# Performance work log

Measured on AMD Instinct MI355X. Metric: run time of the kernel, lower is better.

Reference implementation:

```python
import jax, jax.numpy as jnp
import numpy as np

B, SEQ, DIM = 2, 2048, 1024
HEADS, HEAD_DIM = 16, 64
HIDDEN = 2816
EPS = 1e-5
LN_EPS = 1e-5


def rmsnorm(x, w, eps=EPS):
    return x * jax.lax.rsqrt(jnp.mean(x * x, axis=-1, keepdims=True) + eps) * w


def layernorm(x, w, b, eps=LN_EPS):
    mu = jnp.mean(x, axis=-1, keepdims=True)
    var = jnp.mean((x - mu) ** 2, axis=-1, keepdims=True)
    return (x - mu) * jax.lax.rsqrt(var + eps) * w + b


def modulate(x, shift, scale):
    # x: [B,S,D], shift/scale: [B,D]
    return x * (1.0 + scale[:, None, :]) + shift[:, None, :]


def apply_rope(t, cos, sin):
    # t: [B,S,H,D]; cos/sin: [S, D/2] -> complex multiply on (even,odd) pairs
    t = t.reshape(*t.shape[:-1], HEAD_DIM // 2, 2)
    t0, t1 = t[..., 0], t[..., 1]
    c = cos[None, :, None, :]
    s = sin[None, :, None, :]
    o0 = t0 * c - t1 * s
    o1 = t0 * s + t1 * c
    return jnp.stack([o0, o1], axis=-1).reshape(*t.shape[:-2], HEAD_DIM)


def setup_inputs() -> dict:
    key = jax.random.key(0)
    ks = jax.random.split(key, 12)
    def w(k, shape, s=0.02):
        return jax.random.normal(k, shape, dtype=jnp.float32) * s
    x = jax.random.normal(ks[0], (B, SEQ, DIM), dtype=jnp.float32)
    adaln_input = jax.random.normal(ks[1], (B, DIM), dtype=jnp.float32)
    pos = jnp.arange(SEQ, dtype=jnp.float32)
    inv_freq = 1.0 / (10000.0 ** (jnp.arange(0, HEAD_DIM, 2, dtype=jnp.float32) / HEAD_DIM))
    ang = pos[:, None] * inv_freq[None, :]  # [S, D/2]
    return dict(
        x=x, adaln_input=adaln_input,
        freqs_cos=jnp.cos(ang), freqs_sin=jnp.sin(ang),
        wq=w(ks[2], (DIM, DIM)), wk=w(ks[3], (DIM, DIM)),
        wv=w(ks[4], (DIM, DIM)), wo=w(ks[5], (DIM, DIM)),
        q_norm_w=jnp.ones(DIM, jnp.float32), q_norm_b=jnp.zeros(DIM, jnp.float32),
        k_norm_w=jnp.ones(DIM, jnp.float32), k_norm_b=jnp.zeros(DIM, jnp.float32),
        attn_norm_w=jnp.ones(DIM, jnp.float32), ffn_norm_w=jnp.ones(DIM, jnp.float32),
        ada_w=w(ks[6], (DIM, 6 * DIM)), ada_b=jnp.zeros(6 * DIM, jnp.float32),
        w1=w(ks[7], (DIM, HIDDEN)), w2=w(ks[8], (HIDDEN, DIM)), w3=w(ks[9], (DIM, HIDDEN)),
    )


def reference(x, adaln_input, freqs_cos, freqs_sin, wq, wk, wv, wo,
              q_norm_w, q_norm_b, k_norm_w, k_norm_b,
              attn_norm_w, ffn_norm_w, ada_w, ada_b, w1, w2, w3):
    # adaLN modulation: SiLU -> Linear -> 6 chunks of [B, DIM]
    m = jax.nn.silu(adaln_input) @ ada_w + ada_b
    shift_msa, scale_msa, gate_msa, shift_mlp, scale_mlp, gate_mlp = jnp.split(m, 6, axis=1)

    # --- attention branch ---
    h = modulate(rmsnorm(x, attn_norm_w), shift_msa, scale_msa)
    xq = layernorm(h @ wq, q_norm_w, q_norm_b)
    xk = layernorm(h @ wk, k_norm_w, k_norm_b)
    xv = h @ wv
    xq = xq.reshape(B, SEQ, HEADS, HEAD_DIM)
    xk = xk.reshape(B, SEQ, HEADS, HEAD_DIM)
    xv = xv.reshape(B, SEQ, HEADS, HEAD_DIM)
    xq = apply_rope(xq, freqs_cos, freqs_sin)
    xk = apply_rope(xk, freqs_cos, freqs_sin)
    scale = 1.0 / jnp.sqrt(jnp.float32(HEAD_DIM))
    scores = jnp.einsum('bshd,bthd->bhst', xq, xk) * scale  # [B,H,S,S]
    probs = jax.nn.softmax(scores, axis=-1)
    attn = jnp.einsum('bhst,bthd->bshd', probs, xv).reshape(B, SEQ, DIM)
    attn = attn @ wo
    x = x + gate_msa[:, None, :] * attn

    # --- MLP branch (SwiGLU) ---
    h = modulate(rmsnorm(x, ffn_norm_w), shift_mlp, scale_mlp)
    ffn = (jax.nn.silu(h @ w1) * (h @ w3)) @ w2
    x = x + gate_mlp[:, None, :] * ffn
    return x
```

## Files before the change

kernel.cpp:

```cpp
#include <hip/hip_runtime.h>
#include <hip/hip_bf16.h>

#define B_   2
#define S_   2048
#define D_   1024
#define H_   16
#define HD_  64
#define HID_ 2816

typedef unsigned short u16;
typedef unsigned int   u32;
typedef __attribute__((ext_vector_type(8))) short short8;
typedef __attribute__((ext_vector_type(4))) float f32x4;
typedef __attribute__((ext_vector_type(4))) u32   u32x4;

static __device__ __forceinline__ float bf2f(u16 u){ return __uint_as_float(((u32)u)<<16); }
static __device__ __forceinline__ u16 f2bf(float f){
  u32 u = __float_as_uint(f);
  u32 r = (u + 0x7FFFu + ((u>>16)&1u)) >> 16;
  return (u16)r;
}
static __device__ __forceinline__ u16 f2bfr(float f){
  return (u16)((__float_as_uint(f) + 0x8000u) >> 16);
}
static __device__ __forceinline__ u32 pk2(float a, float b){
  return ((__float_as_uint(a) + 0x8000u) >> 16) | ((__float_as_uint(b) + 0x8000u) & 0xFFFF0000u);
}

static __device__ __forceinline__ void ld4(const u16* p, float* v){
  ushort4 t = *reinterpret_cast<const ushort4*>(p);
  v[0]=bf2f(t.x); v[1]=bf2f(t.y); v[2]=bf2f(t.z); v[3]=bf2f(t.w);
}
static __device__ __forceinline__ void ld4(const float* p, float* v){
  float4 t = *reinterpret_cast<const float4*>(p);
  v[0]=t.x; v[1]=t.y; v[2]=t.z; v[3]=t.w;
}
static __device__ __forceinline__ void st4(u16* p, const float* v){
  ushort4 t; t.x=f2bf(v[0]); t.y=f2bf(v[1]); t.z=f2bf(v[2]); t.w=f2bf(v[3]);
  *reinterpret_cast<ushort4*>(p)=t;
}

static __device__ __forceinline__ float ld1g(const void* p, size_t i, bool f32){
  return f32 ? ((const float*)p)[i] : bf2f(((const u16*)p)[i]);
}
static __device__ __forceinline__ void ld4g(const void* p, size_t i, float* v, bool f32){
  if(f32){
    float4 t = *reinterpret_cast<const float4*>((const float*)p + i);
    v[0]=t.x; v[1]=t.y; v[2]=t.z; v[3]=t.w;
  }else{
    ushort4 t = *reinterpret_cast<const ushort4*>((const u16*)p + i);
    v[0]=bf2f(t.x); v[1]=bf2f(t.y); v[2]=bf2f(t.z); v[3]=bf2f(t.w);
  }
}
static __device__ __forceinline__ void st4g(void* p, size_t i, const float* v, bool f32){
  if(f32){
    float4 t; t.x=v[0]; t.y=v[1]; t.z=v[2]; t.w=v[3];
    *reinterpret_cast<float4*>((float*)p + i) = t;
  }else{
    st4((u16*)p + i, v);
  }
}

static __device__ __forceinline__ void gl2lds16(const u16* g, const u16* l){
  typedef __attribute__((address_space(3))) u16 lds_u16;
  typedef const __attribute__((address_space(1))) u16 glb_u16;
  __builtin_amdgcn_global_load_lds((glb_u16*)(uintptr_t)g,
                                   (lds_u16*)(u32)(uintptr_t)l, 16, 0, 0);
}

__global__ __launch_bounds__(256) void k_probe_zero(const u16* fc_raw, int* flag, float* m){
  int i = blockIdx.x*256 + threadIdx.x;
  if(i < 12288) m[i] = 0.f;
  if(i == 0) *flag = (fc_raw[0]==0) ? 1 : 0;
}

static __device__ __forceinline__ float blk_sum(float v, float* red){
  #pragma unroll
  for(int o=32;o;o>>=1) v += __shfl_xor(v,o,64);
  int lane = threadIdx.x & 63, w = threadIdx.x >> 6;
  if(lane==0) red[w]=v;
  __syncthreads();
  float t = red[0]+red[1]+red[2]+red[3];
  __syncthreads();
  return t;
}

__global__ __launch_bounds__(256) void k_adaln(const void* a, const void* W, const void* bias,
                                               float* m, const int* flag){
  bool f32 = flag[0] != 0;
  __shared__ float sl[2][128];
  int bk = blockIdx.y;
  {
    int bb = threadIdx.x >> 7, kk = threadIdx.x & 127;
    float x = ld1g(a, bb*D_ + bk*128 + kk, f32);
    sl[bb][kk] = x/(1.f+__expf(-x));
  }
  __syncthreads();
  int n = blockIdx.x*256 + threadIdx.x;
  float p0 = 0.f, p1 = 0.f;
  for(int kk=0;kk<128;kk++){
    float w = ld1g(W, (size_t)(bk*128+kk)*6144 + n, f32);
    p0 += sl[0][kk]*w; p1 += sl[1][kk]*w;
  }
  if(bk==0){ float bv = ld1g(bias, n, f32); p0 += bv; p1 += bv; }
  atomicAdd(&m[n], p0);
  atomicAdd(&m[6144+n], p1);
}

__global__ __launch_bounds__(256) void k_rms_mod(const void* x, const void* nw, const float* m,
                                                 u16* h, int shift_off, int scale_off,
                                                 const int* flag){
  bool f32 = flag[0] != 0;
  __shared__ float red[4];
  int row = blockIdx.x; int b = row >> 11;
  int d0 = threadIdx.x*4;
  float v[4]; ld4g(x, (size_t)row*D_ + d0, v, f32);
  float ss = v[0]*v[0]+v[1]*v[1]+v[2]*v[2]+v[3]*v[3];
  float tot = blk_sum(ss, red);
  float r = rsqrtf(tot*(1.f/D_) + 1e-5f);
  const float* mb = m + b*6144;
  float wn[4]; ld4g(nw, d0, wn, f32);
  float o[4];
  #pragma unroll
  for(int j=0;j<4;j++){
    int d = d0+j;
    o[j] = v[j]*r*wn[j]*(1.f+mb[scale_off+d]) + mb[shift_off+d];
  }
  st4(h + (size_t)row*D_ + d0, o);
}

__global__ __launch_bounds__(256) void k_resid_rms(const void* x, const u16* y, const float* m,
                                                   const void* nw, float* x2, u16* h,
                                                   const int* flag){
  bool f32 = flag[0] != 0;
  __shared__ float red[4];
  int row = blockIdx.x; int b = row >> 11;
  int d0 = threadIdx.x*4;
  size_t i4 = (size_t)row*D_ + d0;
  float xv[4], yv[4];
  ld4g(x, i4, xv, f32); ld4(y+i4, yv);
  const float* mb = m + b*6144;
  float v[4];
  #pragma unroll
  for(int j=0;j<4;j++) v[j] = xv[j] + mb[2048+d0+j]*yv[j];
  float4 t; t.x=v[0]; t.y=v[1]; t.z=v[2]; t.w=v[3];
  *reinterpret_cast<float4*>(x2+i4) = t;
  float ss = v[0]*v[0]+v[1]*v[1]+v[2]*v[2]+v[3]*v[3];
  float tot = blk_sum(ss, red);
  float r = rsqrtf(tot*(1.f/D_) + 1e-5f);
  float wn[4]; ld4g(nw, d0, wn, f32);
  float o[4];
  #pragma unroll
  for(int j=0;j<4;j++)
    o[j] = v[j]*r*wn[j]*(1.f+mb[4096+d0+j]) + mb[3072+d0+j];
  st4(h + i4, o);
}

__global__ __launch_bounds__(256) void k_ln_rope2(u16* t, const void* qw, const void* qb,
                                                  const void* kw, const void* kb2,
                                                  const void* fc, const void* fs, const int* flag){
  bool f32 = flag[0] != 0;
  __shared__ float red[4];
  int row = blockIdx.x; int s = row & (S_-1);
  const void* w  = blockIdx.y ? kw  : qw;
  const void* bb = blockIdx.y ? kb2 : qb;
  int d0 = threadIdx.x*4;
  u16* tp = t + (size_t)row*3072 + blockIdx.y*1024 + d0;
  float v[4]; ld4(tp, v);
  float sm = v[0]+v[1]+v[2]+v[3];
  float sq = v[0]*v[0]+v[1]*v[1]+v[2]*v[2]+v[3]*v[3];
  float tsm = blk_sum(sm, red);
  float tsq = blk_sum(sq, red);
  float mu  = tsm*(1.f/D_);
  float var = tsq*(1.f/D_) - mu*mu;
  float rs  = rsqrtf(var + 1e-5f);
  float wv[4], bv[4]; ld4g(w, d0, wv, f32); ld4g(bb, d0, bv, f32);
  float y[4];
  #pragma unroll
  for(int j=0;j<4;j++) y[j] = (v[j]-mu)*rs*wv[j] + bv[j];
  int pos = d0 & 63; int i0 = pos>>1;
  float c0 = ld1g(fc, s*32+i0,   f32), s0 = ld1g(fs, s*32+i0,   f32);
  float c1 = ld1g(fc, s*32+i0+1, f32), s1 = ld1g(fs, s*32+i0+1, f32);
  float o[4];
  o[0] = y[0]*c0 - y[1]*s0;
  o[1] = y[0]*s0 + y[1]*c0;
  o[2] = y[2]*c1 - y[3]*s1;
  o[3] = y[2]*s1 + y[3]*c1;
  st4(tp, o);
}

__global__ __launch_bounds__(256) void k_wt3(const void* W0, const void* W1, const void* W2,
                                             u16* WT, int Kd, int Nd, const int* flag){
  bool f32 = flag[0] != 0;
  const void* W = blockIdx.z==0 ? W0 : (blockIdx.z==1 ? W1 : W2);
  u16* dst_base = WT + (size_t)blockIdx.z * (size_t)Kd * Nd;
  __shared__ u16 L[64][72];
  int tid = threadIdx.x;
  int k0 = blockIdx.x*64, n0 = blockIdx.y*64;
  int r = tid>>2, c0 = (tid&3)*16;
  if(f32){
    const float* Wf = (const float*)W;
    #pragma unroll
    for(int j=0;j<4;j++){
      float4 t = *reinterpret_cast<const float4*>(&Wf[(size_t)(k0+r)*Nd + n0 + c0 + j*4]);
      L[r][c0+j*4+0]=f2bfr(t.x); L[r][c0+j*4+1]=f2bfr(t.y);
      L[r][c0+j*4+2]=f2bfr(t.z); L[r][c0+j*4+3]=f2bfr(t.w);
    }
  }else{
    const u16* Wh = (const u16*)W;
    *reinterpret_cast<short8*>(&L[r][c0]) =
      *reinterpret_cast<const short8*>(&Wh[(size_t)(k0+r)*Nd + n0 + c0]);
    *reinterpret_cast<short8*>(&L[r][c0+8]) =
      *reinterpret_cast<const short8*>(&Wh[(size_t)(k0+r)*Nd + n0 + c0 + 8]);
  }
  __syncthreads();
  int n = tid>>2, kk0 = (tid&3)*16;
  u16 tmp[16];
  #pragma unroll
  for(int j=0;j<16;j++) tmp[j] = L[kk0+j][n];
  u16* dst = dst_base + (size_t)(n0+n)*Kd + k0 + kk0;
  *reinterpret_cast<short8*>(dst)   = *reinterpret_cast<const short8*>(tmp);
  *reinterpret_cast<short8*>(dst+8) = *reinterpret_cast<const short8*>(tmp+8);
}

__global__ __launch_bounds__(256) void k_wt13(const void* W1, const void* W3,
                                              u16* WT, const int* flag){
  bool f32 = flag[0] != 0;
  const int Kd = 1024, Nd = HID_;
  const void* W = blockIdx.z ? W3 : W1;
  int radd = blockIdx.z ? 32 : 0;
  __shared__ u16 L[64][72];
  int tid = threadIdx.x;
  int k0 = blockIdx.x*64, n0 = blockIdx.y*64;
  int r = tid>>2, c0 = (tid&3)*16;
  if(f32){
    const float* Wf = (const float*)W;
    #pragma unroll
    for(int j=0;j<4;j++){
      float4 t = *reinterpret_cast<const float4*>(&Wf[(size_t)(k0+r)*Nd + n0 + c0 + j*4]);
      L[r][c0+j*4+0]=f2bfr(t.x); L[r][c0+j*4+1]=f2bfr(t.y);
      L[r][c0+j*4+2]=f2bfr(t.z); L[r][c0+j*4+3]=f2bfr(t.w);
    }
  }else{
    const u16* Wh = (const u16*)W;
    *reinterpret_cast<short8*>(&L[r][c0]) =
      *reinterpret_cast<const short8*>(&Wh[(size_t)(k0+r)*Nd + n0 + c0]);
    *reinterpret_cast<short8*>(&L[r][c0+8]) =
      *reinterpret_cast<const short8*>(&Wh[(size_t)(k0+r)*Nd + n0 + c0 + 8]);
  }
  __syncthreads();
  int n = tid>>2, kk0 = (tid&3)*16;
  u16 tmp[16];
  #pragma unroll
  for(int j=0;j<16;j++) tmp[j] = L[kk0+j][n];
  int nglob = n0 + n;
  int rw = ((nglob>>5)<<6) + (nglob&31) + radd;
  u16* dst = WT + (size_t)rw*Kd + k0 + kk0;
  *reinterpret_cast<short8*>(dst)   = *reinterpret_cast<const short8*>(tmp);
  *reinterpret_cast<short8*>(dst+8) = *reinterpret_cast<const short8*>(tmp+8);
}

template<int TM, int EPI>
__global__ __launch_bounds__(256) void k_gemm_mfma(const u16* A, int lda, const u16* BT, int ldb,
                                                   u16* C, int N, int K,
                                                   const float* x2, const float* mg,
                                                   void* outp, const int* flag){
  __shared__ __align__(16) u16 As[TM*64];
  __shared__ __align__(16) u16 Bs[128*64];
  int tid = threadIdx.x, lane = tid&63, w = tid>>6;
  int col = lane&15, quad = lane>>4;
  int row0 = blockIdx.y*TM, col0 = blockIdx.x*128;
  const u16* Ab = A  + (size_t)row0*lda;
  const u16* Bb = BT + (size_t)col0*ldb;
  constexpr int MI = TM/32;
  int wm = (w>>1)*(TM/2);
  int wn = (w&1)*64;
  f32x4 acc[MI][4];
  #pragma unroll
  for(int i=0;i<MI;i++)
    #pragma unroll
    for(int j=0;j<4;j++) acc[i][j] = (f32x4){0.f,0.f,0.f,0.f};

  for(int k0=0;k0<K;k0+=64){
    __syncthreads();
    #pragma unroll
    for(int i=0;i<TM/32;i++){
      int c = i*256 + w*64 + lane;
      int r = c>>3, s = c&7, gs = s ^ (r&7);
      gl2lds16(Ab + (size_t)r*lda + k0 + gs*8, As + (size_t)c*8);
    }
    #pragma unroll
    for(int i=0;i<4;i++){
      int c = i*256 + w*64 + lane;
      int r = c>>3, s = c&7, gs = s ^ (r&7);
      gl2lds16(Bb + (size_t)r*ldb + k0 + gs*8, Bs + (size_t)c*8);
    }
    __syncthreads();
    #pragma unroll
    for(int ks=0;ks<64;ks+=32){
      short8 af[MI], bfr[4];
      #pragma unroll
      for(int mi=0;mi<MI;mi++){
        int r = wm+mi*16+col;
        int sch = ((ks>>3) + quad) ^ (col&7);
        af[mi] = *reinterpret_cast<const short8*>(&As[r*64 + sch*8]);
      }
      #pragma unroll
      for(int ni=0;ni<4;ni++){
        int r = wn+ni*16+col;
        int sch = ((ks>>3) + quad) ^ (col&7);
        bfr[ni] = *reinterpret_cast<const short8*>(&Bs[r*64 + sch*8]);
      }
      #pragma unroll
      for(int mi=0;mi<MI;mi++)
        #pragma unroll
        for(int ni=0;ni<4;ni++)
          acc[mi][ni] = __builtin_amdgcn_mfma_f32_16x16x32_bf16(af[mi], bfr[ni], acc[mi][ni], 0,0,0);
    }
  }
  if constexpr(EPI==0){
    #pragma unroll
    for(int mi=0;mi<MI;mi++)
      #pragma unroll
      for(int r=0;r<4;r++){
        size_t rowoff = (size_t)(row0+wm+mi*16+quad*4+r)*N + col0 + wn;
        #pragma unroll
        for(int ni=0;ni<4;ni++)
          C[rowoff + ni*16 + col] = f2bfr(acc[mi][ni][r]);
      }
  } else if constexpr(EPI==1){
    int cb = blockIdx.x*64 + (wn?32:0) + col;
    #pragma unroll
    for(int mi=0;mi<MI;mi++)
      #pragma unroll
      for(int r=0;r<4;r++){
        int row = row0+wm+mi*16+quad*4+r;
        u16* gp = C + (size_t)row*HID_ + cb;
        #pragma unroll
        for(int ni=0;ni<2;ni++){
          float a = acc[mi][ni][r], cc = acc[mi][ni+2][r];
          float sv = a * __builtin_amdgcn_rcpf(1.f + __builtin_amdgcn_exp2f(-1.4426950f*a));
          gp[ni*16] = f2bfr(sv*cc);
        }
      }
  } else {
    bool f32o = flag[0] != 0;
    #pragma unroll
    for(int mi=0;mi<MI;mi++)
      #pragma unroll
      for(int r=0;r<4;r++){
        int row = row0+wm+mi*16+quad*4+r;
        int b = row >> 11;
        #pragma unroll
        for(int ni=0;ni<4;ni++){
          int cc = col0 + wn + ni*16 + col;
          float v = x2[(size_t)row*D_ + cc] + mg[b*6144 + 5120 + cc]*acc[mi][ni][r];
          if(f32o) ((float*)outp)[(size_t)row*D_ + cc] = v;
          else     ((u16*)outp)[(size_t)row*D_ + cc]   = f2bfr(v);
        }
      }
  }
}

__global__ __launch_bounds__(256) void k_vt(const u16* v, int vstr, u16* vt){
  __shared__ u16 L[64][72];
  int tid = threadIdx.x;
  int wg = blockIdx.x;
  int kblk = wg & 31; int bh = wg >> 5; int h = bh & 15, b = bh >> 4;
  int row = tid>>2, c0 = (tid&3)*16;
  const u16* src = v + (size_t)(b*S_ + kblk*64 + row)*vstr + h*HD_ + c0;
  *reinterpret_cast<short8*>(&L[row][c0])   = *reinterpret_cast<const short8*>(src);
  *reinterpret_cast<short8*>(&L[row][c0+8]) = *reinterpret_cast<const short8*>(src+8);
  __syncthreads();
  int hd = tid>>2, k0 = (tid&3)*16;
  u16 tmp[16];
  #pragma unroll
  for(int j=0;j<16;j++) tmp[j] = L[k0+j][hd];
  u16* dst = vt + ((size_t)bh*HD_ + hd)*S_ + kblk*64 + k0;
  *reinterpret_cast<short8*>(dst)   = *reinterpret_cast<const short8*>(tmp);
  *reinterpret_cast<short8*>(dst+8) = *reinterpret_cast<const short8*>(tmp+8);
}

__global__ __launch_bounds__(256) void k_attn_mfma(const u16* q, const u16* k, const u16* vt,
                                                   u16* o, int qks){
  __shared__ __align__(16) u16 Ks[2][64*72];
  __shared__ __align__(16) u16 Vs[2][64*72];
  int tid = threadIdx.x, lane = tid & 63, wid = tid >> 6;
  int col = lane & 15, quad = lane >> 4;
  int wg = blockIdx.x;
  int qblk = wg & 31; int bh = wg >> 5; int h = bh & 15, b = bh >> 4;

  const u16* kb  = k  + (size_t)b*S_*qks + h*HD_;
  const u16* vtb = vt + (size_t)bh*HD_*S_;

  short8 qa0, qa1;
  {
    const float qscale = 0.18033688f;
    const u16* qp = q + (size_t)(b*S_ + qblk*64 + wid*16 + col)*qks + h*HD_ + quad*8;
    short8 t0 = *reinterpret_cast<const short8*>(qp);
    short8 t1 = *reinterpret_cast<const short8*>(qp + 32);
    #pragma unroll
    for(int j=0;j<8;j++){
      qa0[j] = (short)f2bf(bf2f((u16)t0[j])*qscale);
      qa1[j] = (short)f2bf(bf2f((u16)t1[j])*qscale);
    }
  }
  float m_i = -1e30f, l_i = 0.f;
  f32x4 acc[4];
  #pragma unroll
  for(int t=0;t<4;t++) acc[t] = (f32x4){0.f,0.f,0.f,0.f};

  int l0 = tid>>3,        kc0 = (tid&7)*8;
  int l1 = (256+tid)>>3,  kc1 = ((256+tid)&7)*8;
  int kl0 = 32*(l0>>5) + 8*((l0>>2)&3) + 4*((l0>>4)&1) + (l0&3);
  int kl1 = 32*(l1>>5) + 8*((l1>>2)&3) + 4*((l1>>4)&1) + (l1&3);
  const u16* kp0 = kb + (size_t)kl0*qks + kc0;
  const u16* kp1 = kb + (size_t)kl1*qks + kc1;
  const u16* vp0 = vtb + (size_t)l0*S_ + kc0;
  const u16* vp1 = vtb + (size_t)l1*S_ + kc1;
  int ko0 = l0*72 + kc0, ko1 = l1*72 + kc1;

  {
    *reinterpret_cast<short8*>(&Ks[0][ko0]) = *reinterpret_cast<const short8*>(kp0);
    *reinterpret_cast<short8*>(&Ks[0][ko1]) = *reinterpret_cast<const short8*>(kp1);
    *reinterpret_cast<short8*>(&Vs[0][ko0]) = *reinterpret_cast<const short8*>(vp0);
    *reinterpret_cast<short8*>(&Vs[0][ko1]) = *reinterpret_cast<const short8*>(vp1);
  }

  for(int i=0;i<32;i++){
    __syncthreads();
    const u16* Kc = Ks[i&1];
    const u16* Vc = Vs[i&1];
    short8 nk0, nk1, nv0, nv1;
    bool more = (i < 31);
    if(more){
      size_t t0n = (size_t)(i+1)*64;
      nk0 = *reinterpret_cast<const short8*>(kp0 + t0n*qks);
      nk1 = *reinterpret_cast<const short8*>(kp1 + t0n*qks);
      nv0 = *reinterpret_cast<const short8*>(vp0 + t0n);
      nv1 = *reinterpret_cast<const short8*>(vp1 + t0n);
    }

    f32x4 st[4];
    #pragma unroll
    for(int mt=0;mt<4;mt++){
      st[mt] = (f32x4){0.f,0.f,0.f,0.f};
      short8 ka0 = *reinterpret_cast<const short8*>(&Kc[(mt*16+col)*72 + quad*8]);
      short8 ka1 = *reinterpret_cast<const short8*>(&Kc[(mt*16+col)*72 + 32 + quad*8]);
      st[mt] = __builtin_amdgcn_mfma_f32_16x16x32_bf16(ka0, qa0, st[mt], 0,0,0);
      st[mt] = __builtin_amdgcn_mfma_f32_16x16x32_bf16(ka1, qa1, st[mt], 0,0,0);
    }
    float cm = st[0][0];
    #pragma unroll
    for(int mt=0;mt<4;mt++)
      #pragma unroll
      for(int r=0;r<4;r++) cm = fmaxf(cm, st[mt][r]);
    cm = fmaxf(cm, __shfl_xor(cm,16,64));
    cm = fmaxf(cm, __shfl_xor(cm,32,64));
    if(__any(cm > m_i)){
      float mn = fmaxf(m_i, cm);
      float al = __builtin_amdgcn_exp2f(m_i - mn);
      m_i = mn;
      l_i *= al;
      #pragma unroll
      for(int t=0;t<4;t++) acc[t] *= al;
    }
    float pe[4][4];
    #pragma unroll
    for(int mt=0;mt<4;mt++)
      #pragma unroll
      for(int r=0;r<4;r++) pe[mt][r] = __builtin_amdgcn_exp2f(st[mt][r]-m_i);
    #pragma unroll
    for(int w=0;w<2;w++){
      u32x4 pw;
      pw[0] = pk2(pe[2*w][0],   pe[2*w][1]);
      pw[1] = pk2(pe[2*w][2],   pe[2*w][3]);
      pw[2] = pk2(pe[2*w+1][0], pe[2*w+1][1]);
      pw[3] = pk2(pe[2*w+1][2], pe[2*w+1][3]);
      short8 pb = *reinterpret_cast<short8*>(&pw);
      #pragma unroll
      for(int ht=0;ht<4;ht++){
        short8 vf = *reinterpret_cast<const short8*>(&Vc[(ht*16+col)*72 + w*32 + quad*8]);
        acc[ht] = __builtin_amdgcn_mfma_f32_16x16x32_bf16(vf, pb, acc[ht], 0,0,0);
      }
    }
    float ps = 0.f;
    #pragma unroll
    for(int mt=0;mt<4;mt++)
      #pragma unroll
      for(int r=0;r<4;r++) ps += pe[mt][r];
    ps += __shfl_xor(ps,16,64);
    ps += __shfl_xor(ps,32,64);
    l_i += ps;

    if(more){
      u16* Kn = (u16*)Ks[(i+1)&1];
      u16* Vn = (u16*)Vs[(i+1)&1];
      *reinterpret_cast<short8*>(&Kn[ko0]) = nk0;
      *reinterpret_cast<short8*>(&Kn[ko1]) = nk1;
      *reinterpret_cast<short8*>(&Vn[ko0]) = nv0;
      *reinterpret_cast<short8*>(&Vn[ko1]) = nv1;
    }
  }
  float inv = __builtin_amdgcn_rcpf(l_i);
  u16* ob = o + (size_t)(b*S_ + qblk*64 + wid*16 + col)*D_ + h*HD_;
  #pragma unroll
  for(int ht=0;ht<4;ht++){
    uint2 t;
    t.x = pk2(acc[ht][0]*inv, acc[ht][1]*inv);
    t.y = pk2(acc[ht][2]*inv, acc[ht][3]*inv);
    *reinterpret_cast<uint2*>(ob + ht*16 + quad*4) = t;
  }
}

extern "C" void kernel_launch(void* const* d_in, const int* in_sizes, int n_in,
                              void* d_out, int out_size, void* d_ws, size_t ws_size,
                              hipStream_t stream){
  const void* x   = d_in[0];
  const void* ada = d_in[1];
  const void* fc  = d_in[2];
  const void* fs  = d_in[3];
  const void* wq  = d_in[4];
  const void* wk  = d_in[5];
  const void* wv  = d_in[6];
  const void* wo  = d_in[7];
  const void* qnw = d_in[8];
  const void* qnb = d_in[9];
  const void* knw = d_in[10];
  const void* knb = d_in[11];
  const void* anw = d_in[12];
  const void* fnw = d_in[13];
  const void* aw  = d_in[14];
  const void* ab  = d_in[15];
  const void* w1  = d_in[16];
  const void* w2  = d_in[17];
  const void* w3  = d_in[18];
  char* ws = (char*)d_ws;
  const size_t MB = 1u<<20;

  int*   flag = (int*)ws;
  float* m    = (float*)(ws + 4096);
  u16*  hbuf  = (u16*)(ws + 1*MB);
  u16*  xqkv  = (u16*)(ws + 9*MB);
  float* x2   = (float*)(ws + 9*MB);
  u16*  proj  = (u16*)(ws + 25*MB);
  u16*  wreg  = (u16*)(ws + 33*MB);
  u16*  g     = (u16*)(ws + 45*MB);
  u16*  vt    = wreg;

  dim3 blk(256);

  k_probe_zero<<<dim3(48), blk, 0, stream>>>((const u16*)fc, flag, m);
  k_adaln<<<dim3(24,8), blk, 0, stream>>>(ada, aw, ab, m, flag);
  k_rms_mod<<<dim3(B_*S_), blk, 0, stream>>>(x, anw, m, hbuf, 0, 1024, flag);

  k_wt3<<<dim3(16,16,3), blk, 0, stream>>>(wq, wk, wv, wreg, 1024, 1024, flag);
  k_gemm_mfma<128,0><<<dim3(24,32), blk, 0, stream>>>(hbuf, 1024, wreg, 1024, xqkv,
                                                      3072, 1024, nullptr, nullptr, nullptr, flag);

  k_ln_rope2<<<dim3(B_*S_,2), blk, 0, stream>>>(xqkv, qnw, qnb, knw, knb, fc, fs, flag);
  k_vt<<<dim3(B_*H_*S_/64), blk, 0, stream>>>(xqkv + 2048, 3072, vt);
  k_attn_mfma<<<dim3(B_*H_*S_/64), blk, 0, stream>>>(xqkv, xqkv + 1024, vt, hbuf, 3072);

  k_wt3<<<dim3(16,16,1), blk, 0, stream>>>(wo, wo, wo, wreg, 1024, 1024, flag);
  k_gemm_mfma<64,0><<<dim3(8,64), blk, 0, stream>>>(hbuf, 1024, wreg, 1024, proj,
                                                    1024, 1024, nullptr, nullptr, nullptr, flag);
  k_resid_rms<<<dim3(B_*S_), blk, 0, stream>>>(x, proj, m, fnw, x2, hbuf, flag);

  k_wt13<<<dim3(16,44,2), blk, 0, stream>>>(w1, w3, wreg, flag);
  k_gemm_mfma<128,1><<<dim3(44,32), blk, 0, stream>>>(hbuf, 1024, wreg, 1024, g,
                                                      5632, 1024, nullptr, nullptr, nullptr, flag);
  k_wt3<<<dim3(44,16,1), blk, 0, stream>>>(w2, w2, w2, wreg, 2816, 1024, flag);
  k_gemm_mfma<64,2><<<dim3(8,64), blk, 0, stream>>>(g, 2816, wreg, 2816, nullptr,
                                                    1024, 2816, x2, m, d_out, flag);
}
```

Before: 428.8 us.

## Use direct global-to-LDS loads with XOR swizzle in attention kernel

Replaces register-staged K/V tile prefetch in the flash attention kernel with direct global-to-LDS loads (gl2lds16) into an unpadded, XOR-swizzled shared layout, removing the register round trip and padding. The row max now uses v_max3 and permlane swaps, and the row-sum cross-lane reduction is deferred to after the loop. bf16 packing switches to the hardware v_cvt_pk_bf16_f32 instruction. The change relies on the gl2lds16 helper existing elsewhere in the file, and the async LDS writes must be ordered correctly by the existing barrier.

```diff
diff --git a/kernel.cpp b/kernel.cpp
--- a/kernel.cpp
+++ b/kernel.cpp
@@ -13,6 +13,7 @@
 typedef __attribute__((ext_vector_type(8))) short short8;
 typedef __attribute__((ext_vector_type(4))) float f32x4;
 typedef __attribute__((ext_vector_type(4))) u32   u32x4;
+typedef __attribute__((ext_vector_type(2))) unsigned uvec2;
 
 static __device__ __forceinline__ float bf2f(u16 u){ return __uint_as_float(((u32)u)<<16); }
 static __device__ __forceinline__ u16 f2bf(float f){
@@ -25,6 +26,28 @@
 }
 static __device__ __forceinline__ u32 pk2(float a, float b){
   return ((__float_as_uint(a) + 0x8000u) >> 16) | ((__float_as_uint(b) + 0x8000u) & 0xFFFF0000u);
+}
+static __device__ __forceinline__ u32 cvtpk(float lo, float hi){
+  u32 r; asm("v_cvt_pk_bf16_f32 %0, %1, %2" : "=v"(r) : "v"(lo), "v"(hi)); return r;
+}
+static __device__ __forceinline__ float vmax3(float a, float b, float c){
+  float d; asm("v_max3_f32 %0, %1, %2, %3" : "=v"(d) : "v"(a), "v"(b), "v"(c)); return d;
+}
+static __device__ __forceinline__ void plswap16(float x, float& a, float& b){
+#if __has_builtin(__builtin_amdgcn_permlane16_swap)
+  uvec2 r = __builtin_amdgcn_permlane16_swap(__float_as_uint(x), __float_as_uint(x), false, false);
+  a = __uint_as_float(r[0]); b = __uint_as_float(r[1]);
+#else
+  a = x; b = __shfl_xor(x, 16, 64);
+#endif
+}
+static __device__ __forceinline__ void plswap32(float x, float& a, float& b){
+#if __has_builtin(__builtin_amdgcn_permlane32_swap)
+  uvec2 r = __builtin_amdgcn_permlane32_swap(__float_as_uint(x), __float_as_uint(x), false, false);
+  a = __uint_as_float(r[0]); b = __uint_as_float(r[1]);
+#else
+  a = x; b = __shfl_xor(x, 32, 64);
+#endif
 }
 
 static __device__ __forceinline__ void ld4(const u16* p, float* v){
@@ -383,10 +406,11 @@
 
 __global__ __launch_bounds__(256) void k_attn_mfma(const u16* q, const u16* k, const u16* vt,
                                                    u16* o, int qks){
-  __shared__ __align__(16) u16 Ks[2][64*72];
-  __shared__ __align__(16) u16 Vs[2][64*72];
+  __shared__ __align__(16) u16 Ks[2][64*64];
+  __shared__ __align__(16) u16 Vs[2][64*64];
   int tid = threadIdx.x, lane = tid & 63, wid = tid >> 6;
   int col = lane & 15, quad = lane >> 4;
+  int c7 = col & 7;
   int wg = blockIdx.x;
   int qblk = wg & 31; int bh = wg >> 5; int h = bh & 15, b = bh >> 4;
 
@@ -410,53 +434,52 @@
   #pragma unroll
   for(int t=0;t<4;t++) acc[t] = (f32x4){0.f,0.f,0.f,0.f};
 
-  int l0 = tid>>3,        kc0 = (tid&7)*8;
-  int l1 = (256+tid)>>3,  kc1 = ((256+tid)&7)*8;
+  int l0 = tid>>3;
+  int l1 = 32 + l0;
+  int gs = ((tid&7) ^ (l0&7))*8;
   int kl0 = 32*(l0>>5) + 8*((l0>>2)&3) + 4*((l0>>4)&1) + (l0&3);
   int kl1 = 32*(l1>>5) + 8*((l1>>2)&3) + 4*((l1>>4)&1) + (l1&3);
-  const u16* kp0 = kb + (size_t)kl0*qks + kc0;
-  const u16* kp1 = kb + (size_t)kl1*qks + kc1;
-  const u16* vp0 = vtb + (size_t)l0*S_ + kc0;
-  const u16* vp1 = vtb + (size_t)l1*S_ + kc1;
-  int ko0 = l0*72 + kc0, ko1 = l1*72 + kc1;
-
-  {
-    *reinterpret_cast<short8*>(&Ks[0][ko0]) = *reinterpret_cast<const short8*>(kp0);
-    *reinterpret_cast<short8*>(&Ks[0][ko1]) = *reinterpret_cast<const short8*>(kp1);
-    *reinterpret_cast<short8*>(&Vs[0][ko0]) = *reinterpret_cast<const short8*>(vp0);
-    *reinterpret_cast<short8*>(&Vs[0][ko1]) = *reinterpret_cast<const short8*>(vp1);
-  }
+  const u16* kp0 = kb + (size_t)kl0*qks + gs;
+  const u16* kp1 = kb + (size_t)kl1*qks + gs;
+  const u16* vp0 = vtb + (size_t)l0*S_ + gs;
+  const u16* vp1 = vtb + (size_t)l1*S_ + gs;
+
+  gl2lds16(kp0, &Ks[0][tid*8]);
+  gl2lds16(kp1, &Ks[0][2048 + tid*8]);
+  gl2lds16(vp0, &Vs[0][tid*8]);
+  gl2lds16(vp1, &Vs[0][2048 + tid*8]);
 
   for(int i=0;i<32;i++){
     __syncthreads();
     const u16* Kc = Ks[i&1];
     const u16* Vc = Vs[i&1];
-    short8 nk0, nk1, nv0, nv1;
-    bool more = (i < 31);
-    if(more){
-      size_t t0n = (size_t)(i+1)*64;
-      nk0 = *reinterpret_cast<const short8*>(kp0 + t0n*qks);
-      nk1 = *reinterpret_cast<const short8*>(kp1 + t0n*qks);
-      nv0 = *reinterpret_cast<const short8*>(vp0 + t0n);
-      nv1 = *reinterpret_cast<const short8*>(vp1 + t0n);
+    if(i < 31){
+      size_t off = (size_t)(i+1)*64;
+      u16* Kn = (u16*)Ks[(i+1)&1];
+      u16* Vn = (u16*)Vs[(i+1)&1];
+      gl2lds16(kp0 + off*qks, &Kn[tid*8]);
+      gl2lds16(kp1 + off*qks, &Kn[2048 + tid*8]);
+      gl2lds16(vp0 + off,     &Vn[tid*8]);
+      gl2lds16(vp1 + off,     &Vn[2048 + tid*8]);
     }
 
     f32x4 st[4];
     #pragma unroll
     for(int mt=0;mt<4;mt++){
       st[mt] = (f32x4){0.f,0.f,0.f,0.f};
-      short8 ka0 = *reinterpret_cast<const short8*>(&Kc[(mt*16+col)*72 + quad*8]);
-      short8 ka1 = *reinterpret_cast<const short8*>(&Kc[(mt*16+col)*72 + 32 + quad*8]);
+      short8 ka0 = *reinterpret_cast<const short8*>(&Kc[(mt*16+col)*64 + ((quad  ) ^ c7)*8]);
+      short8 ka1 = *reinterpret_cast<const short8*>(&Kc[(mt*16+col)*64 + ((quad+4) ^ c7)*8]);
       st[mt] = __builtin_amdgcn_mfma_f32_16x16x32_bf16(ka0, qa0, st[mt], 0,0,0);
       st[mt] = __builtin_amdgcn_mfma_f32_16x16x32_bf16(ka1, qa1, st[mt], 0,0,0);
     }
-    float cm = st[0][0];
-    #pragma unroll
-    for(int mt=0;mt<4;mt++)
-      #pragma unroll
-      for(int r=0;r<4;r++) cm = fmaxf(cm, st[mt][r]);
-    cm = fmaxf(cm, __shfl_xor(cm,16,64));
-    cm = fmaxf(cm, __shfl_xor(cm,32,64));
+    float t0 = vmax3(st[0][0], st[0][1], st[0][2]);
+    float t1 = vmax3(st[0][3], st[1][0], st[1][1]);
+    float t2 = vmax3(st[1][2], st[1][3], st[2][0]);
+    float t3 = vmax3(st[2][1], st[2][2], st[2][3]);
+    float t4 = vmax3(st[3][0], st[3][1], st[3][2]);
+    float cm = fmaxf(vmax3(t0, t1, t2), vmax3(t3, t4, st[3][3]));
+    { float a, bb2; plswap16(cm, a, bb2); cm = fmaxf(a, bb2);
+      plswap32(cm, a, bb2); cm = fmaxf(a, bb2); }
     if(__any(cm > m_i)){
       float mn = fmaxf(m_i, cm);
       float al = __builtin_amdgcn_exp2f(m_i - mn);
@@ -473,42 +496,32 @@
     #pragma unroll
     for(int w=0;w<2;w++){
       u32x4 pw;
-      pw[0] = pk2(pe[2*w][0],   pe[2*w][1]);
-      pw[1] = pk2(pe[2*w][2],   pe[2*w][3]);
-      pw[2] = pk2(pe[2*w+1][0], pe[2*w+1][1]);
-      pw[3] = pk2(pe[2*w+1][2], pe[2*w+1][3]);
+      pw[0] = cvtpk(pe[2*w][0],   pe[2*w][1]);
+      pw[1] = cvtpk(pe[2*w][2],   pe[2*w][3]);
+      pw[2] = cvtpk(pe[2*w+1][0], pe[2*w+1][1]);
+      pw[3] = cvtpk(pe[2*w+1][2], pe[2*w+1][3]);
       short8 pb = *reinterpret_cast<short8*>(&pw);
       #pragma unroll
       for(int ht=0;ht<4;ht++){
-        short8 vf = *reinterpret_cast<const short8*>(&Vc[(ht*16+col)*72 + w*32 + quad*8]);
+        short8 vf = *reinterpret_cast<const short8*>(&Vc[(ht*16+col)*64 + ((w*4+quad) ^ c7)*8]);
         acc[ht] = __builtin_amdgcn_mfma_f32_16x16x32_bf16(vf, pb, acc[ht], 0,0,0);
       }
     }
-    float ps = 0.f;
-    #pragma unroll
-    for(int mt=0;mt<4;mt++)
-      #pragma unroll
-      for(int r=0;r<4;r++) ps += pe[mt][r];
-    ps += __shfl_xor(ps,16,64);
-    ps += __shfl_xor(ps,32,64);
-    l_i += ps;
-
-    if(more){
-      u16* Kn = (u16*)Ks[(i+1)&1];
-      u16* Vn = (u16*)Vs[(i+1)&1];
-      *reinterpret_cast<short8*>(&Kn[ko0]) = nk0;
-      *reinterpret_cast<short8*>(&Kn[ko1]) = nk1;
-      *reinterpret_cast<short8*>(&Vn[ko0]) = nv0;
-      *reinterpret_cast<short8*>(&Vn[ko1]) = nv1;
-    }
-  }
+    float s0 = (pe[0][0]+pe[0][1]) + (pe[0][2]+pe[0][3]);
+    float s1 = (pe[1][0]+pe[1][1]) + (pe[1][2]+pe[1][3]);
+    float s2 = (pe[2][0]+pe[2][1]) + (pe[2][2]+pe[2][3]);
+    float s3 = (pe[3][0]+pe[3][1]) + (pe[3][2]+pe[3][3]);
+    l_i += (s0+s1) + (s2+s3);
+  }
+  { float a, bb2; plswap16(l_i, a, bb2); l_i = a + bb2;
+    plswap32(l_i, a, bb2); l_i = a + bb2; }
   float inv = __builtin_amdgcn_rcpf(l_i);
   u16* ob = o + (size_t)(b*S_ + qblk*64 + wid*16 + col)*D_ + h*HD_;
   #pragma unroll
   for(int ht=0;ht<4;ht++){
     uint2 t;
-    t.x = pk2(acc[ht][0]*inv, acc[ht][1]*inv);
-    t.y = pk2(acc[ht][2]*inv, acc[ht][3]*inv);
+    t.x = cvtpk(acc[ht][0]*inv, acc[ht][1]*inv);
+    t.y = cvtpk(acc[ht][2]*inv, acc[ht][3]*inv);
     *reinterpret_cast<uint2*>(ob + ht*16 + quad*4) = t;
   }
 }
```

Measured after the change: 442.0 us. 3.1% more time.
